# Performance work log

Hardware: AMD Instinct MI355X
Metric: run time of the kernel (lower is better)

## Reference

```python
import jax, jax.numpy as jnp
import numpy as np

IN_DIM = 512
POS_RFACTOR = 8
MAX_POS = 128
WP = MAX_POS // POS_RFACTOR  # pooled 1D width = 16


def _sin_table(max_len, d):
    # HANet-style sinusoidal table; row 0 is all zeros
    pos = np.arange(max_len)[:, None].astype(np.float64)
    j = np.arange(d)[None, :]
    angle = pos / np.power(10000.0, 2 * (j // 2) / d)
    enc = np.zeros((max_len, d), dtype=np.float32)
    enc[1:, 0::2] = np.sin(angle[1:, 0::2])
    enc[1:, 1::2] = np.cos(angle[1:, 1::2])
    return jnp.asarray(enc)


def setup_inputs() -> dict:
    key = jax.random.key(0)
    ks = jax.random.split(key, 6)
    B, C, H, W = 4, IN_DIM, 64, 64
    Ck = C // 2
    s = 1.0 / np.sqrt(C)
    return {
        "x": jax.random.normal(ks[0], (B, C, H, W), jnp.float32),
        "Wq": jax.random.normal(ks[1], (Ck, C), jnp.float32) * s,
        "bq": jnp.zeros((Ck,), jnp.float32),
        "Wk": jax.random.normal(ks[2], (Ck, C), jnp.float32) * s,
        "bk": jnp.zeros((Ck,), jnp.float32),
        "Wv": jax.random.normal(ks[3], (C, C), jnp.float32) * s,
        "bv": jnp.zeros((C,), jnp.float32),
        "gamma": jnp.ones((1,), jnp.float32),  # torch inits to 0; nonzero here so output/grads are non-trivial
        "pe_table": _sin_table(MAX_POS, C),
        "pos": jax.random.randint(ks[4], (B, H, W), 0, MAX_POS, dtype=jnp.int32),
    }


def reference(x, Wq, bq, Wk, bk, Wv, bv, gamma, pe_table, pos):
    B, C, H, W = x.shape
    # colpool: AdaptiveAvgPool2d((1, WP)) -> mean over H, block-mean over W (W % WP == 0)
    x1d = x.mean(axis=2).reshape(B, C, WP, W // WP).mean(axis=-1)  # B,C,WP
    # PosEncoding1D (eval mode, no noise): select first row, //rfactor, nearest-resize to WP, embed
    p = pos[:, 0, :] // POS_RFACTOR                 # B,W
    nidx = (jnp.arange(WP) * W) // WP               # nearest-neighbor indices
    pe = pe_table[p[:, nidx]]                       # B,WP,C
    x1d = x1d + jnp.transpose(pe, (0, 2, 1))        # B,C,WP
    # Upsample(x1d.unsqueeze(2), (H,W)): bilinear align_corners=True; height dim is 1 -> constant
    src = jnp.arange(W, dtype=jnp.float32) * (WP - 1) / (W - 1)
    i0 = jnp.floor(src).astype(jnp.int32)
    i1 = jnp.minimum(i0 + 1, WP - 1)
    t = (src - i0.astype(jnp.float32)).astype(x.dtype)
    row = x1d[:, :, i0] * (1.0 - t) + x1d[:, :, i1] * t  # B,C,W
    x2d = jnp.broadcast_to(row[:, :, None, :], (B, C, H, W))
    # 1x1 conv projections
    q = jnp.einsum('bchw,oc->bohw', x, Wq) + bq[None, :, None, None]
    k = jnp.einsum('bchw,oc->bohw', x2d, Wk) + bk[None, :, None, None]
    v = jnp.einsum('bchw,oc->bohw', x, Wv) + bv[None, :, None, None]
    N = H * W
    q = q.reshape(B, -1, N)   # B,Ck,N
    k = k.reshape(B, -1, N)   # B,Ck,N
    v = v.reshape(B, C, N)    # B,C,N
    energy = jnp.einsum('bcn,bcm->bnm', q, k)        # B,N,N (query n, key m), unscaled
    attn = jax.nn.softmax(energy, axis=-1)
    out = jnp.einsum('bcm,bnm->bcn', v, attn)        # B,C,N
    out = out.reshape(B, C, H, W)
    return gamma[0] * out + x
```

## Files before the change

kernel.cpp:

```cpp
#include <hip/hip_runtime.h>

#define CDIM 512
#define OKD  256
#define NDIM 4096
#define NT   32

#define OFF_XMH 0
#define OFF_X1  131072
#define OFF_K1  163840
#define OFF_M1  180224
#define OFF_CB1 212992
#define OFF_VMB 213056

typedef float f32x4  __attribute__((ext_vector_type(4)));
typedef short shortx4 __attribute__((ext_vector_type(4)));
typedef short shortx8 __attribute__((ext_vector_type(8)));
typedef unsigned short ushortx4 __attribute__((ext_vector_type(4)));

static __device__ __forceinline__ unsigned short f2bf(float f) {
  unsigned u = __float_as_uint(f);
  u = (u + 0x7FFFu + ((u >> 16) & 1u)) >> 16;
  return (unsigned short)u;
}

__global__ __launch_bounds__(256) void k_reduce(const float* __restrict__ x,
                                                const float* __restrict__ pe,
                                                const int* __restrict__ pos,
                                                float* __restrict__ xmh,
                                                float* __restrict__ x1pe) {
  int t = threadIdx.x;
  int bc = blockIdx.x * 4 + (t >> 6);
  int w4 = t & 15;
  int hoff = (t >> 4) & 3;
  const float4* xp = (const float4*)(x) + (size_t)bc * (64 * 16);
  float4 acc = make_float4(0.f, 0.f, 0.f, 0.f);
#pragma unroll
  for (int k = 0; k < 16; ++k) {
    float4 v = xp[(hoff + 4 * k) * 16 + w4];
    acc.x += v.x; acc.y += v.y; acc.z += v.z; acc.w += v.w;
  }
  acc.x += __shfl_xor(acc.x, 16); acc.y += __shfl_xor(acc.y, 16);
  acc.z += __shfl_xor(acc.z, 16); acc.w += __shfl_xor(acc.w, 16);
  acc.x += __shfl_xor(acc.x, 32); acc.y += __shfl_xor(acc.y, 32);
  acc.z += __shfl_xor(acc.z, 32); acc.w += __shfl_xor(acc.w, 32);
  if (hoff == 0) {
    const float inv = 1.f / 64.f;
    float4 o = make_float4(acc.x * inv, acc.y * inv, acc.z * inv, acc.w * inv);
    ((float4*)xmh)[bc * 16 + w4] = o;
    int b = bc >> 9;
    int c = bc & 511;
    int ps = pos[b * 4096 + 4 * w4] >> 3;
    float x1 = (o.x + o.y + o.z + o.w) * 0.25f + pe[ps * CDIM + c];
    x1pe[bc * 16 + w4] = x1;
  }
}

__global__ __launch_bounds__(256) void k_vmk1(const float* __restrict__ Wv,
                                              const float* __restrict__ bv,
                                              const float* __restrict__ Wk,
                                              const float* __restrict__ bk,
                                              const float* __restrict__ xmh,
                                              const float* __restrict__ x1pe,
                                              unsigned short* __restrict__ vmb,
                                              float* __restrict__ K1) {
  __shared__ float xsh[64][68];
  int t = threadIdx.x;
  int blk = blockIdx.x;
  if (blk < 128) {
    int b = blk >> 5;
    int c0 = (blk & 31) * 16;
    int c = c0 + (t >> 4);
    int wq = t & 15;
    const float* Wr = Wv + c * CDIM;
    float a0 = 0.f, a1 = 0.f, a2 = 0.f, a3 = 0.f;
    int cpl = t >> 2, quad = t & 3;
    for (int cp0 = 0; cp0 < CDIM; cp0 += 64) {
      __syncthreads();
#pragma unroll
      for (int rr = 0; rr < 4; ++rr) {
        *(float4*)&xsh[cpl][quad * 16 + rr * 4] =
            *(const float4*)&xmh[((size_t)(b * CDIM + cp0 + cpl)) * 64 + quad * 16 + rr * 4];
      }
      __syncthreads();
#pragma unroll 8
      for (int cp = 0; cp < 64; ++cp) {
        float wv = Wr[cp0 + cp];
        float4 xv = *(const float4*)&xsh[cp][wq * 4];
        a0 += wv * xv.x; a1 += wv * xv.y; a2 += wv * xv.z; a3 += wv * xv.w;
      }
    }
    float bb = bv[c];
    ushortx4 pu;
    pu.x = f2bf(a0 + bb); pu.y = f2bf(a1 + bb); pu.z = f2bf(a2 + bb); pu.w = f2bf(a3 + bb);
    *(ushortx4*)&vmb[((size_t)(b * CDIM + c)) * 64 + wq * 4] = pu;
  } else {
    int idx = blk - 128;
    int b = idx >> 4;
    int o = (idx & 15) * 16 + (t >> 4);
    int i = t & 15;
    const float* Wr = Wk + o * CDIM;
    const float* xb = x1pe + (b << 9) * 16 + i;
    float acc = bk[o];
#pragma unroll 8
    for (int c = 0; c < CDIM; ++c) acc += Wr[c] * xb[c * 16];
    K1[((b << 8) + o) * 16 + i] = acc;
  }
}

__global__ __launch_bounds__(256) void k_m1(const float* __restrict__ Wq,
                                            const float* __restrict__ bq,
                                            const float* __restrict__ K1,
                                            float* __restrict__ M1,
                                            float* __restrict__ cb1) {
  int t = threadIdx.x;
  int blk = blockIdx.x;
  if (blk < 128) {
    int b = blk >> 5;
    int c = (blk & 31) * 16 + (t >> 4);
    int i = t & 15;
    const float* Wc = Wq + c;
    const float* Kb = K1 + (b << 8) * 16 + i;
    float acc = 0.f;
#pragma unroll 8
    for (int o = 0; o < OKD; ++o) acc += Wc[o * CDIM] * Kb[o * 16];
    M1[((b << 9) + c) * 16 + i] = acc;
  } else if (t < 64) {
    int b = t >> 4, i = t & 15;
    const float* Kb = K1 + (b << 8) * 16 + i;
    float acc = 0.f;
    for (int o = 0; o < OKD; ++o) acc += bq[o] * Kb[o * 16];
    cb1[b * 16 + i] = acc;
  }
}

__global__ __launch_bounds__(512, 4) void k_attn(const float* __restrict__ x,
                                                 const float* __restrict__ M1,
                                                 const float* __restrict__ cb1,
                                                 const unsigned short* __restrict__ vmb,
                                                 const float* __restrict__ gamma,
                                                 float* __restrict__ out) {
  __shared__ __align__(16) char smem[55296];
  float* m1f = (float*)smem;
  float (*xs)[36] = (float (*)[36])(smem + 32768);
  float* e1p = (float*)smem;
  char* p_t = smem + 51200;

  const int t = threadIdx.x;
  const int lane = t & 63;
  const int b = blockIdx.x >> 7;
  const int n0 = (blockIdx.x & 127) * NT;

  {
    const float4* src = (const float4*)(M1 + (b << 13));
    float4* dst = (float4*)m1f;
#pragma unroll
    for (int k2 = 0; k2 < 4; ++k2) dst[t + k2 * 512] = src[t + k2 * 512];
  }

  const int q  = t & 7;
  const int ig = (t >> 3) & 3;
  const int cg = t >> 5;
  float acc[4][4] = {};
  for (int ch = 0; ch < 4; ++ch) {
    const int c0 = ch * 128;
    if (ch) __syncthreads();
    {
      const int c_l = t >> 2, nq = t & 3;
      const float* gp = x + (size_t)(b * CDIM + c0 + c_l) * NDIM + n0 + nq * 8;
      float4 v0 = *(const float4*)gp;
      float4 v1 = *(const float4*)(gp + 4);
      *(float4*)&xs[c_l][nq * 8]     = v0;
      *(float4*)&xs[c_l][nq * 8 + 4] = v1;
    }
    __syncthreads();
#pragma unroll
    for (int cc = 0; cc < 8; ++cc) {
      const int c_l = cg * 8 + cc;
      float4 x4 = *(const float4*)&xs[c_l][q * 4];
      float4 m4 = *(const float4*)&m1f[(c0 + c_l) * 16 + ig * 4];
      acc[0][0] += x4.x * m4.x; acc[0][1] += x4.x * m4.y; acc[0][2] += x4.x * m4.z; acc[0][3] += x4.x * m4.w;
      acc[1][0] += x4.y * m4.x; acc[1][1] += x4.y * m4.y; acc[1][2] += x4.y * m4.z; acc[1][3] += x4.y * m4.w;
      acc[2][0] += x4.z * m4.x; acc[2][1] += x4.z * m4.y; acc[2][2] += x4.z * m4.z; acc[2][3] += x4.z * m4.w;
      acc[3][0] += x4.w * m4.x; acc[3][1] += x4.w * m4.y; acc[3][2] += x4.w * m4.z; acc[3][3] += x4.w * m4.w;
    }
  }
  __syncthreads();
#pragma unroll
  for (int jn = 0; jn < 4; ++jn) {
    float4 w4 = make_float4(acc[jn][0], acc[jn][1], acc[jn][2], acc[jn][3]);
    *(float4*)&e1p[(cg * 32 + q * 4 + jn) * 20 + ig * 4] = w4;
  }
  __syncthreads();

  {
    const int sn = t >> 4;
    const int si = t & 15;
    float ev = cb1[b * 16 + si];
#pragma unroll
    for (int g = 0; g < 16; ++g) ev += e1p[g * 640 + sn * 20 + si];
    float pv[4];
    float mx = -3.4e38f;
#pragma unroll
    for (int j = 0; j < 4; ++j) {
      int w = si * 4 + j;
      float srcf = (float)w * (15.0f / 63.0f);
      int i0 = (int)srcf;
      float tf = srcf - (float)i0;
      int i1 = i0 + 1; if (i1 > 15) i1 = 15;
      float v0 = __shfl(ev, (lane & 48) | i0);
      float v1 = __shfl(ev, (lane & 48) | i1);
      float vv = v0 * (1.0f - tf) + v1 * tf;
      pv[j] = vv;
      mx = fmaxf(mx, vv);
    }
    mx = fmaxf(mx, __shfl_xor(mx, 1));
    mx = fmaxf(mx, __shfl_xor(mx, 2));
    mx = fmaxf(mx, __shfl_xor(mx, 4));
    mx = fmaxf(mx, __shfl_xor(mx, 8));
    float s = 0.f;
#pragma unroll
    for (int j = 0; j < 4; ++j) { pv[j] = __expf(pv[j] - mx); s += pv[j]; }
    s += __shfl_xor(s, 1); s += __shfl_xor(s, 2);
    s += __shfl_xor(s, 4); s += __shfl_xor(s, 8);
    float inv = 1.0f / s;
    ushortx4 pu;
    pu.x = f2bf(pv[0] * inv); pu.y = f2bf(pv[1] * inv);
    pu.z = f2bf(pv[2] * inv); pu.w = f2bf(pv[3] * inv);
    *(ushortx4*)(p_t + sn * 128 + ((si ^ (sn & 15)) << 3)) = pu;
  }
  __syncthreads();

  {
    const int wid = t >> 6;
    const float gm = gamma[0];
    const int nrel = lane & 15;
    const int kg = lane >> 4;
#pragma unroll
    for (int j = 0; j < 8; ++j) {
      const int idx = wid * 8 + j;
      const int ct = idx >> 1, nt = idx & 1;
      f32x4 dacc = {0.f, 0.f, 0.f, 0.f};
      const unsigned short* vrow =
          vmb + ((size_t)(b * CDIM + ct * 16 + nrel)) * 64 + kg * 4;
      const char* prow = p_t + (nt * 16 + nrel) * 128;
#pragma unroll
      for (int ks = 0; ks < 2; ++ks) {
        shortx4 a0 = *(const shortx4*)(vrow + ks * 32);
        shortx4 a1 = *(const shortx4*)(vrow + ks * 32 + 16);
        shortx8 av = __builtin_shufflevector(a0, a1, 0, 1, 2, 3, 4, 5, 6, 7);
        int G0 = (ks * 8 + kg) ^ nrel;
        int G1 = (ks * 8 + 4 + kg) ^ nrel;
        shortx4 b0 = *(const shortx4*)(prow + G0 * 8);
        shortx4 b1 = *(const shortx4*)(prow + G1 * 8);
        shortx8 bv2 = __builtin_shufflevector(b0, b1, 0, 1, 2, 3, 4, 5, 6, 7);
        dacc = __builtin_amdgcn_mfma_f32_16x16x32_bf16(av, bv2, dacc, 0, 0, 0);
      }
#pragma unroll
      for (int r = 0; r < 4; ++r) {
        int c_o = ct * 16 + kg * 4 + r;
        size_t base = (size_t)(b * CDIM + c_o) * NDIM + n0 + nt * 16 + nrel;
        out[base] = gm * dacc[r] + x[base];
      }
    }
  }
}

extern "C" void kernel_launch(void* const* d_in, const int* in_sizes, int n_in,
                              void* d_out, int out_size, void* d_ws, size_t ws_size,
                              hipStream_t stream) {
  const float* x     = (const float*)d_in[0];
  const float* Wq    = (const float*)d_in[1];
  const float* bq    = (const float*)d_in[2];
  const float* Wk    = (const float*)d_in[3];
  const float* bk    = (const float*)d_in[4];
  const float* Wv    = (const float*)d_in[5];
  const float* bv    = (const float*)d_in[6];
  const float* gamma = (const float*)d_in[7];
  const float* pe    = (const float*)d_in[8];
  const int*   pos   = (const int*)d_in[9];
  float* out = (float*)d_out;
  float* ws  = (float*)d_ws;

  float* xmh  = ws + OFF_XMH;
  float* x1pe = ws + OFF_X1;
  float* K1   = ws + OFF_K1;
  float* M1   = ws + OFF_M1;
  float* cb1  = ws + OFF_CB1;
  unsigned short* vmb = (unsigned short*)(ws + OFF_VMB);

  hipLaunchKernelGGL(k_reduce, dim3(512), dim3(256), 0, stream, x, pe, pos, xmh, x1pe);
  hipLaunchKernelGGL(k_vmk1, dim3(192), dim3(256), 0, stream, Wv, bv, Wk, bk, xmh, x1pe, vmb, K1);
  hipLaunchKernelGGL(k_m1, dim3(129), dim3(256), 0, stream, Wq, bq, K1, M1, cb1);
  hipLaunchKernelGGL(k_attn, dim3(512), dim3(512), 0, stream, x, M1, cb1, vmb, gamma, out);
}
```

Baseline: 149.1 us.

## Move energy and V projection GEMMs onto bf16 MFMA with prepacked M1 layout

The per-block x·M1 energy product in the attention kernel now uses bf16 MFMA instructions, with M1 stored by k_m1 in bf16 already laid out as MFMA A-fragments. This removes the LDS staging of M1 and x and the scalar FMA loop. The Wv·xmh projection is also converted to MFMA, and the K1 and M1 dot products get split accumulators. In exchange, x and Wv are now rounded to bf16 before these products, which loses precision, and x is read with strided scalar global loads.

```diff
diff --git a/kernel.cpp b/kernel.cpp
--- a/kernel.cpp
+++ b/kernel.cpp
@@ -3,24 +3,25 @@
 #define CDIM 512
 #define OKD  256
 #define NDIM 4096
-#define NT   32
 
 #define OFF_XMH 0
 #define OFF_X1  131072
 #define OFF_K1  163840
-#define OFF_M1  180224
-#define OFF_CB1 212992
-#define OFF_VMB 213056
+#define OFF_M1A 180224
+#define OFF_CB1 196608
+#define OFF_VMB 196672
 
 typedef float f32x4  __attribute__((ext_vector_type(4)));
 typedef short shortx4 __attribute__((ext_vector_type(4)));
 typedef short shortx8 __attribute__((ext_vector_type(8)));
-typedef unsigned short ushortx4 __attribute__((ext_vector_type(4)));
 
 static __device__ __forceinline__ unsigned short f2bf(float f) {
   unsigned u = __float_as_uint(f);
   u = (u + 0x7FFFu + ((u >> 16) & 1u)) >> 16;
   return (unsigned short)u;
+}
+static __device__ __forceinline__ unsigned pk2(float lo, float hi) {
+  return (unsigned)f2bf(lo) | ((unsigned)f2bf(hi) << 16);
 }
 
 __global__ __launch_bounds__(256) void k_reduce(const float* __restrict__ x,
@@ -55,7 +56,7 @@
   }
 }
 
-__global__ __launch_bounds__(256) void k_vmk1(const float* __restrict__ Wv,
+__global__ __launch_bounds__(128) void k_vmk1(const float* __restrict__ Wv,
                                               const float* __restrict__ bv,
                                               const float* __restrict__ Wk,
                                               const float* __restrict__ bk,
@@ -63,54 +64,62 @@
                                               const float* __restrict__ x1pe,
                                               unsigned short* __restrict__ vmb,
                                               float* __restrict__ K1) {
-  __shared__ float xsh[64][68];
   int t = threadIdx.x;
   int blk = blockIdx.x;
-  if (blk < 128) {
-    int b = blk >> 5;
-    int c0 = (blk & 31) * 16;
-    int c = c0 + (t >> 4);
-    int wq = t & 15;
-    const float* Wr = Wv + c * CDIM;
+  if (blk < 64) {
+    int wid = blk * 2 + (t >> 6);
+    int lane = t & 63, nrel = lane & 15, kg = lane >> 4;
+    int b = wid >> 5, rem = wid & 31, cgrp = rem >> 2, wt = rem & 3;
+    f32x4 acc[4] = {{0,0,0,0},{0,0,0,0},{0,0,0,0},{0,0,0,0}};
+    for (int kt = 0; kt < 16; ++kt) {
+      const float* xp = xmh + (size_t)(b * 512 + kt * 32 + kg * 4) * 64 + wt * 16 + nrel;
+      float v0 = xp[0], v1 = xp[64], v2 = xp[128], v3 = xp[192];
+      float v4 = xp[1024], v5 = xp[1088], v6 = xp[1152], v7 = xp[1216];
+      shortx8 bf;
+      unsigned* bu = (unsigned*)&bf;
+      bu[0] = pk2(v0, v1); bu[1] = pk2(v2, v3);
+      bu[2] = pk2(v4, v5); bu[3] = pk2(v6, v7);
+#pragma unroll
+      for (int m = 0; m < 4; ++m) {
+        int c = (cgrp * 4 + m) * 16 + nrel;
+        const float* wp = Wv + (size_t)c * 512 + kt * 32 + kg * 4;
+        float4 a0 = *(const float4*)wp;
+        float4 a1 = *(const float4*)(wp + 16);
+        shortx8 af;
+        unsigned* au = (unsigned*)&af;
+        au[0] = pk2(a0.x, a0.y); au[1] = pk2(a0.z, a0.w);
+        au[2] = pk2(a1.x, a1.y); au[3] = pk2(a1.z, a1.w);
+        acc[m] = __builtin_amdgcn_mfma_f32_16x16x32_bf16(af, bf, acc[m], 0, 0, 0);
+      }
+    }
+#pragma unroll
+    for (int m = 0; m < 4; ++m)
+#pragma unroll
+      for (int r = 0; r < 4; ++r) {
+        int c = (cgrp * 4 + m) * 16 + kg * 4 + r;
+        vmb[(size_t)(b * 512 + c) * 64 + wt * 16 + nrel] = f2bf(acc[m][r] + bv[c]);
+      }
+  } else {
+    int idx = blk - 64;
+    int b = idx >> 5, og = idx & 31;
+    int o = og * 8 + (t >> 4), i = t & 15;
+    const float* Wr = Wk + (size_t)o * 512;
+    const float* xb = x1pe + ((size_t)b * 512) * 16 + i;
     float a0 = 0.f, a1 = 0.f, a2 = 0.f, a3 = 0.f;
-    int cpl = t >> 2, quad = t & 3;
-    for (int cp0 = 0; cp0 < CDIM; cp0 += 64) {
-      __syncthreads();
-#pragma unroll
-      for (int rr = 0; rr < 4; ++rr) {
-        *(float4*)&xsh[cpl][quad * 16 + rr * 4] =
-            *(const float4*)&xmh[((size_t)(b * CDIM + cp0 + cpl)) * 64 + quad * 16 + rr * 4];
-      }
-      __syncthreads();
-#pragma unroll 8
-      for (int cp = 0; cp < 64; ++cp) {
-        float wv = Wr[cp0 + cp];
-        float4 xv = *(const float4*)&xsh[cp][wq * 4];
-        a0 += wv * xv.x; a1 += wv * xv.y; a2 += wv * xv.z; a3 += wv * xv.w;
-      }
-    }
-    float bb = bv[c];
-    ushortx4 pu;
-    pu.x = f2bf(a0 + bb); pu.y = f2bf(a1 + bb); pu.z = f2bf(a2 + bb); pu.w = f2bf(a3 + bb);
-    *(ushortx4*)&vmb[((size_t)(b * CDIM + c)) * 64 + wq * 4] = pu;
-  } else {
-    int idx = blk - 128;
-    int b = idx >> 4;
-    int o = (idx & 15) * 16 + (t >> 4);
-    int i = t & 15;
-    const float* Wr = Wk + o * CDIM;
-    const float* xb = x1pe + (b << 9) * 16 + i;
-    float acc = bk[o];
-#pragma unroll 8
-    for (int c = 0; c < CDIM; ++c) acc += Wr[c] * xb[c * 16];
-    K1[((b << 8) + o) * 16 + i] = acc;
+    for (int c = 0; c < 512; c += 4) {
+      a0 += Wr[c]     * xb[c * 16];
+      a1 += Wr[c + 1] * xb[(c + 1) * 16];
+      a2 += Wr[c + 2] * xb[(c + 2) * 16];
+      a3 += Wr[c + 3] * xb[(c + 3) * 16];
+    }
+    K1[((b << 8) + o) * 16 + i] = bk[o] + a0 + a1 + a2 + a3;
   }
 }
 
 __global__ __launch_bounds__(256) void k_m1(const float* __restrict__ Wq,
                                             const float* __restrict__ bq,
                                             const float* __restrict__ K1,
-                                            float* __restrict__ M1,
+                                            unsigned short* __restrict__ m1A,
                                             float* __restrict__ cb1) {
   int t = threadIdx.x;
   int blk = blockIdx.x;
@@ -120,10 +129,18 @@
     int i = t & 15;
     const float* Wc = Wq + c;
     const float* Kb = K1 + (b << 8) * 16 + i;
-    float acc = 0.f;
-#pragma unroll 8
-    for (int o = 0; o < OKD; ++o) acc += Wc[o * CDIM] * Kb[o * 16];
-    M1[((b << 9) + c) * 16 + i] = acc;
+    float a0 = 0.f, a1 = 0.f, a2 = 0.f, a3 = 0.f;
+    for (int o = 0; o < OKD; o += 4) {
+      a0 += Wc[o * CDIM]       * Kb[o * 16];
+      a1 += Wc[(o + 1) * CDIM] * Kb[(o + 1) * 16];
+      a2 += Wc[(o + 2) * CDIM] * Kb[(o + 2) * 16];
+      a3 += Wc[(o + 3) * CDIM] * Kb[(o + 3) * 16];
+    }
+    float acc = a0 + a1 + a2 + a3;
+    int kt = c >> 5, kl = c & 31;
+    int kg = (kl < 16) ? (kl >> 2) : ((kl - 16) >> 2);
+    int j  = (kl & 3) + ((kl < 16) ? 0 : 4);
+    m1A[(size_t)b * 8192 + ((kt * 16 + i) * 4 + kg) * 8 + j] = f2bf(acc);
   } else if (t < 64) {
     int b = t >> 4, i = t & 15;
     const float* Kb = K1 + (b << 8) * 16 + i;
@@ -134,61 +151,47 @@
 }
 
 __global__ __launch_bounds__(512, 4) void k_attn(const float* __restrict__ x,
-                                                 const float* __restrict__ M1,
+                                                 const unsigned short* __restrict__ m1A,
                                                  const float* __restrict__ cb1,
                                                  const unsigned short* __restrict__ vmb,
                                                  const float* __restrict__ gamma,
                                                  float* __restrict__ out) {
-  __shared__ __align__(16) char smem[55296];
-  float* m1f = (float*)smem;
-  float (*xs)[36] = (float (*)[36])(smem + 32768);
-  float* e1p = (float*)smem;
-  char* p_t = smem + 51200;
+  __shared__ float e1w[8][32][17];
+  __shared__ __align__(16) char p_t[4096];
 
   const int t = threadIdx.x;
   const int lane = t & 63;
-  const int b = blockIdx.x >> 7;
-  const int n0 = (blockIdx.x & 127) * NT;
+  const int wv = t >> 6;
+  const int b  = blockIdx.x >> 7;
+  const int n0 = (blockIdx.x & 127) * 32;
+  const int nrel = lane & 15;
+  const int kg = lane >> 4;
 
   {
-    const float4* src = (const float4*)(M1 + (b << 13));
-    float4* dst = (float4*)m1f;
-#pragma unroll
-    for (int k2 = 0; k2 < 4; ++k2) dst[t + k2 * 512] = src[t + k2 * 512];
-  }
-
-  const int q  = t & 7;
-  const int ig = (t >> 3) & 3;
-  const int cg = t >> 5;
-  float acc[4][4] = {};
-  for (int ch = 0; ch < 4; ++ch) {
-    const int c0 = ch * 128;
-    if (ch) __syncthreads();
-    {
-      const int c_l = t >> 2, nq = t & 3;
-      const float* gp = x + (size_t)(b * CDIM + c0 + c_l) * NDIM + n0 + nq * 8;
-      float4 v0 = *(const float4*)gp;
-      float4 v1 = *(const float4*)(gp + 4);
-      *(float4*)&xs[c_l][nq * 8]     = v0;
-      *(float4*)&xs[c_l][nq * 8 + 4] = v1;
-    }
-    __syncthreads();
-#pragma unroll
-    for (int cc = 0; cc < 8; ++cc) {
-      const int c_l = cg * 8 + cc;
-      float4 x4 = *(const float4*)&xs[c_l][q * 4];
-      float4 m4 = *(const float4*)&m1f[(c0 + c_l) * 16 + ig * 4];
-      acc[0][0] += x4.x * m4.x; acc[0][1] += x4.x * m4.y; acc[0][2] += x4.x * m4.z; acc[0][3] += x4.x * m4.w;
-      acc[1][0] += x4.y * m4.x; acc[1][1] += x4.y * m4.y; acc[1][2] += x4.y * m4.z; acc[1][3] += x4.y * m4.w;
-      acc[2][0] += x4.z * m4.x; acc[2][1] += x4.z * m4.y; acc[2][2] += x4.z * m4.z; acc[2][3] += x4.z * m4.w;
-      acc[3][0] += x4.w * m4.x; acc[3][1] += x4.w * m4.y; acc[3][2] += x4.w * m4.z; acc[3][3] += x4.w * m4.w;
-    }
-  }
-  __syncthreads();
-#pragma unroll
-  for (int jn = 0; jn < 4; ++jn) {
-    float4 w4 = make_float4(acc[jn][0], acc[jn][1], acc[jn][2], acc[jn][3]);
-    *(float4*)&e1p[(cg * 32 + q * 4 + jn) * 20 + ig * 4] = w4;
+    f32x4 pacc[2] = {{0,0,0,0},{0,0,0,0}};
+#pragma unroll
+    for (int ktw = 0; ktw < 2; ++ktw) {
+      int ktg = wv * 2 + ktw;
+      shortx8 af = *(const shortx8*)(m1A + (size_t)b * 8192 +
+                                     ((size_t)((ktg * 16 + nrel) * 4 + kg)) * 8);
+#pragma unroll
+      for (int nt = 0; nt < 2; ++nt) {
+        const float* xp = x + (size_t)(b * 512 + wv * 64 + ktw * 32 + kg * 4) * NDIM +
+                          n0 + nt * 16 + nrel;
+        float v0 = xp[0],          v1 = xp[NDIM],        v2 = xp[2 * NDIM],  v3 = xp[3 * NDIM];
+        float v4 = xp[16 * NDIM],  v5 = xp[17 * NDIM],   v6 = xp[18 * NDIM], v7 = xp[19 * NDIM];
+        shortx8 bf;
+        unsigned* bu = (unsigned*)&bf;
+        bu[0] = pk2(v0, v1); bu[1] = pk2(v2, v3);
+        bu[2] = pk2(v4, v5); bu[3] = pk2(v6, v7);
+        pacc[nt] = __builtin_amdgcn_mfma_f32_16x16x32_bf16(af, bf, pacc[nt], 0, 0, 0);
+      }
+    }
+#pragma unroll
+    for (int nt = 0; nt < 2; ++nt)
+#pragma unroll
+      for (int r = 0; r < 4; ++r)
+        e1w[wv][nt * 16 + nrel][kg * 4 + r] = pacc[nt][r];
   }
   __syncthreads();
 
@@ -197,7 +200,7 @@
     const int si = t & 15;
     float ev = cb1[b * 16 + si];
 #pragma unroll
-    for (int g = 0; g < 16; ++g) ev += e1p[g * 640 + sn * 20 + si];
+    for (int g = 0; g < 8; ++g) ev += e1w[g][sn][si];
     float pv[4];
     float mx = -3.4e38f;
 #pragma unroll
@@ -223,21 +226,18 @@
     s += __shfl_xor(s, 1); s += __shfl_xor(s, 2);
     s += __shfl_xor(s, 4); s += __shfl_xor(s, 8);
     float inv = 1.0f / s;
-    ushortx4 pu;
-    pu.x = f2bf(pv[0] * inv); pu.y = f2bf(pv[1] * inv);
-    pu.z = f2bf(pv[2] * inv); pu.w = f2bf(pv[3] * inv);
-    *(ushortx4*)(p_t + sn * 128 + ((si ^ (sn & 15)) << 3)) = pu;
+    unsigned lo = pk2(pv[0] * inv, pv[1] * inv);
+    unsigned hi = pk2(pv[2] * inv, pv[3] * inv);
+    unsigned* dst = (unsigned*)(p_t + sn * 128 + ((si ^ (sn & 15)) << 3));
+    dst[0] = lo; dst[1] = hi;
   }
   __syncthreads();
 
   {
-    const int wid = t >> 6;
     const float gm = gamma[0];
-    const int nrel = lane & 15;
-    const int kg = lane >> 4;
 #pragma unroll
     for (int j = 0; j < 8; ++j) {
-      const int idx = wid * 8 + j;
+      const int idx = wv * 8 + j;
       const int ct = idx >> 1, nt = idx & 1;
       f32x4 dacc = {0.f, 0.f, 0.f, 0.f};
       const unsigned short* vrow =
@@ -284,12 +284,12 @@
   float* xmh  = ws + OFF_XMH;
   float* x1pe = ws + OFF_X1;
   float* K1   = ws + OFF_K1;
-  float* M1   = ws + OFF_M1;
+  unsigned short* m1A = (unsigned short*)(ws + OFF_M1A);
   float* cb1  = ws + OFF_CB1;
   unsigned short* vmb = (unsigned short*)(ws + OFF_VMB);
 
   hipLaunchKernelGGL(k_reduce, dim3(512), dim3(256), 0, stream, x, pe, pos, xmh, x1pe);
-  hipLaunchKernelGGL(k_vmk1, dim3(192), dim3(256), 0, stream, Wv, bv, Wk, bk, xmh, x1pe, vmb, K1);
-  hipLaunchKernelGGL(k_m1, dim3(129), dim3(256), 0, stream, Wq, bq, K1, M1, cb1);
-  hipLaunchKernelGGL(k_attn, dim3(512), dim3(512), 0, stream, x, M1, cb1, vmb, gamma, out);
-}
+  hipLaunchKernelGGL(k_vmk1, dim3(192), dim3(128), 0, stream, Wv, bv, Wk, bk, xmh, x1pe, vmb, K1);
+  hipLaunchKernelGGL(k_m1, dim3(129), dim3(256), 0, stream, Wq, bq, K1, m1A, cb1);
+  hipLaunchKernelGGL(k_attn, dim3(512), dim3(512), 0, stream, x, m1A, cb1, vmb, gamma, out);
+}
```

Measured after the change: 138.0 us. 7.4% less time.
